# Kernel tuning notes

Measured on AMD Instinct MI355X. Metric: run time of the kernel, lower is better.

## Reference

```python
import jax, jax.numpy as jnp
import numpy as np

N_NODES = 50000
N_EDGES = 800000
IN_FEAT = 128
HEADS = 4
UNITS = 16
LEAKY_ALPHA = 0.2  # tf.nn.leaky_relu default


def setup_inputs() -> dict:
    key = jax.random.key(0)
    k1, k2, k3, k4, k5 = jax.random.split(key, 5)
    x = jax.random.normal(k1, (N_NODES, IN_FEAT), dtype=jnp.float32)
    edge_index = jax.random.randint(k2, (N_EDGES, 2), 0, N_NODES, dtype=jnp.int32)
    # Dense kernel (glorot-ish scaling), no bias (use_bias=False)
    W = jax.random.normal(k3, (IN_FEAT, HEADS * UNITS), dtype=jnp.float32) * (1.0 / np.sqrt(IN_FEAT))
    glorot = np.sqrt(2.0 / (1 + UNITS)).astype(np.float32)
    att_w1 = jax.random.normal(k4, (HEADS, 1, UNITS), dtype=jnp.float32) * glorot
    att_w2 = jax.random.normal(k5, (HEADS, 1, UNITS), dtype=jnp.float32) * glorot
    return {"x": x, "edge_index": edge_index, "W": W, "att_w1": att_w1, "att_w2": att_w2}


def reference(x, edge_index, W, att_w1, att_w2):
    n_nodes = x.shape[0]
    h = x @ W  # [N, H*U]
    snd_idx = edge_index[:, 0]
    rcv_idx = edge_index[:, 1]
    # gather per-edge features, split into heads -> [H, E, U]
    sender = h[snd_idx].reshape(-1, HEADS, UNITS).transpose(1, 0, 2)
    receiver = h[rcv_idx].reshape(-1, HEADS, UNITS).transpose(1, 0, 2)
    # per-edge, per-head attention logits [H, E]
    att = jnp.sum(att_w1 * sender, axis=-1) + jnp.sum(att_w2 * receiver, axis=-1)
    att = jnp.where(att > 0, att, LEAKY_ALPHA * att)
    # segment softmax over receiver neighborhoods, per head
    seg_max = jax.vmap(lambda a: jax.ops.segment_max(a, rcv_idx, num_segments=n_nodes))(att)  # [H, N]
    e = jnp.exp(att - seg_max[:, rcv_idx])
    denom = jax.vmap(lambda a: jax.ops.segment_sum(a, rcv_idx, num_segments=n_nodes))(e)  # [H, N]
    alpha = e / denom[:, rcv_idx]  # [H, E]
    # weighted scatter-sum of sender features -> [H, N, U]
    out = jax.vmap(lambda v: jax.ops.segment_sum(v, rcv_idx, num_segments=n_nodes))(sender * alpha[:, :, None])
    # concat heads -> [N, H*U]; activation is None (identity)
    return out.transpose(1, 0, 2).reshape(n_nodes, HEADS * UNITS)
```

## Files before the change

### kernel.cpp

```cpp
#include <hip/hip_runtime.h>
#include <math.h>

#define N_NODES 50000
#define N_EDGES 800000
#define IN_FEAT 128
#define HEADS   4
#define UNITS   16
#define OUTF    64
#define LEAKY   0.2f

#define NB      196
#define BCAP    5120
#define GEMM_BLKS 782
#define A_BLOCKS  391
#define EPB     8

typedef __attribute__((ext_vector_type(8))) short bf16x8;
typedef __attribute__((ext_vector_type(4))) float f32x4;

__device__ __forceinline__ unsigned short f2bf(float f) {
    unsigned u = __float_as_uint(f);
    unsigned r = u + 0x7FFFu + ((u >> 16) & 1u);
    return (unsigned short)(r >> 16);
}

union SharedU {
    struct { unsigned short xl[64 * 136]; unsigned short wt[64 * 136]; } g;
    struct { int2 stage[2048]; int hist[256], s[256], excl[256],
             gbase[256], cur[256]; } a;
};

__global__ __launch_bounds__(256) void wt_prep(const float* __restrict__ W,
                                               unsigned short* __restrict__ Wt_g,
                                               int* __restrict__ bucket_cnt) {
    int idx = blockIdx.x * 256 + threadIdx.x;
    if (blockIdx.x == 0 && threadIdx.x < NB) bucket_cnt[threadIdx.x] = 0;
    if (idx < IN_FEAT * OUTF) {
        int k = idx >> 6, c = idx & 63;
        Wt_g[c * IN_FEAT + k] = f2bf(W[idx]);
    }
}

__global__ __launch_bounds__(256) void fused_gemm_bucketA(const float* __restrict__ x,
                                                          const unsigned short* __restrict__ Wt_g,
                                                          const float* __restrict__ w1,
                                                          const float* __restrict__ w2,
                                                          const int2* __restrict__ ei,
                                                          unsigned short* __restrict__ hg,
                                                          float* __restrict__ a1,
                                                          float* __restrict__ a2,
                                                          int* __restrict__ bucket_cnt,
                                                          int2* __restrict__ buckets) {
    __shared__ SharedU sh;
    const int t = threadIdx.x;

    if (blockIdx.x >= GEMM_BLKS) {
        const int e0 = (blockIdx.x - GEMM_BLKS) * 2048;
        sh.a.hist[t] = 0;
        __syncthreads();

        int2 ed[EPB]; int bk[EPB];
        #pragma unroll
        for (int j = 0; j < EPB; ++j) {
            int e = e0 + t + j * 256;
            if (e < N_EDGES) {
                ed[j] = ei[e];
                bk[j] = ed[j].y >> 8;
                atomicAdd(&sh.a.hist[bk[j]], 1);
            } else bk[j] = -1;
        }
        __syncthreads();
        int v = sh.a.hist[t];
        sh.a.s[t] = v;
        __syncthreads();
        #pragma unroll
        for (int off = 1; off < 256; off <<= 1) {
            int u = (t >= off) ? sh.a.s[t - off] : 0;
            __syncthreads();
            sh.a.s[t] += u;
            __syncthreads();
        }
        sh.a.excl[t] = sh.a.s[t] - v;
        sh.a.cur[t] = 0;
        if (t < NB) sh.a.gbase[t] = atomicAdd(&bucket_cnt[t], v);
        __syncthreads();
        #pragma unroll
        for (int j = 0; j < EPB; ++j) {
            if (bk[j] >= 0) {
                int p = sh.a.excl[bk[j]] + atomicAdd(&sh.a.cur[bk[j]], 1);
                sh.a.stage[p] = ed[j];
            }
        }
        __syncthreads();
        const int total = min(2048, N_EDGES - e0);
        for (int i = t; i < total; i += 256) {
            int2 vv = sh.a.stage[i];
            int b = vv.y >> 8;
            buckets[(size_t)b * BCAP + sh.a.gbase[b] + (i - sh.a.excl[b])] = vv;
        }
        return;
    }

    const int node0 = blockIdx.x * 64;
    unsigned short* xl = sh.g.xl;
    unsigned short* wt = sh.g.wt;

    #pragma unroll
    for (int it = 0; it < 8; ++it) {
        int idx = t + 256 * it;
        int r = idx >> 5, q = idx & 31;
        int node = node0 + r;
        float4 v = make_float4(0.f, 0.f, 0.f, 0.f);
        if (node < N_NODES) v = *(const float4*)(x + (size_t)node * IN_FEAT + q * 4);
        ushort4 b;
        b.x = f2bf(v.x); b.y = f2bf(v.y); b.z = f2bf(v.z); b.w = f2bf(v.w);
        *(ushort4*)&xl[r * 136 + q * 4] = b;
    }
    {
        const ushort4* Wt4 = (const ushort4*)Wt_g;
        #pragma unroll
        for (int it = 0; it < 8; ++it) {
            int idx = t + 256 * it;
            int c = idx >> 5, u = idx & 31;
            *(ushort4*)&wt[c * 136 + u * 4] = Wt4[idx];
        }
    }
    __syncthreads();

    const int lane = t & 63, wv = t >> 6;
    const int m = lane & 15, quad = lane >> 4;
    const int n0 = wv * 16;

    f32x4 acc[4] = {{0,0,0,0},{0,0,0,0},{0,0,0,0},{0,0,0,0}};
    #pragma unroll
    for (int kc = 0; kc < 4; ++kc) {
        bf16x8 af = *(bf16x8*)&xl[(n0 + m) * 136 + kc * 32 + quad * 8];
        #pragma unroll
        for (int ct = 0; ct < 4; ++ct) {
            bf16x8 bfr = *(bf16x8*)&wt[(ct * 16 + m) * 136 + kc * 32 + quad * 8];
            acc[ct] = __builtin_amdgcn_mfma_f32_16x16x32_bf16(af, bfr, acc[ct], 0, 0, 0);
        }
    }

    #pragma unroll
    for (int ct = 0; ct < 4; ++ct) {
        const float u1 = w1[ct * 16 + m];
        const float u2 = w2[ct * 16 + m];
        #pragma unroll
        for (int r = 0; r < 4; ++r) {
            float p1 = acc[ct][r] * u1;
            float p2 = acc[ct][r] * u2;
            p1 += __shfl_xor(p1, 1, 64); p1 += __shfl_xor(p1, 2, 64);
            p1 += __shfl_xor(p1, 4, 64); p1 += __shfl_xor(p1, 8, 64);
            p2 += __shfl_xor(p2, 1, 64); p2 += __shfl_xor(p2, 2, 64);
            p2 += __shfl_xor(p2, 4, 64); p2 += __shfl_xor(p2, 8, 64);
            if (m == 0) {
                int node = node0 + n0 + quad * 4 + r;
                if (node < N_NODES) {
                    a1[node * 4 + ct] = p1;
                    a2[node * 4 + ct] = p2;
                }
            }
        }
    }

    __syncthreads();
    unsigned short* hl = sh.g.xl;
    #pragma unroll
    for (int ct = 0; ct < 4; ++ct)
        #pragma unroll
        for (int r = 0; r < 4; ++r)
            hl[(n0 + quad * 4 + r) * 72 + ct * 16 + m] = f2bf(acc[ct][r]);
    __syncthreads();
    #pragma unroll
    for (int it = 0; it < 2; ++it) {
        int u = t + 256 * it;
        int r = u >> 3, cg = u & 7;
        int node = node0 + r;
        if (node < N_NODES)
            *(uint4*)&hg[(size_t)node * OUTF + cg * 8] = *(uint4*)&hl[r * 72 + cg * 8];
    }
}

__global__ __launch_bounds__(256) void bucketB(const int2* __restrict__ buckets,
                                               const int* __restrict__ bucket_cnt,
                                               int* __restrict__ edge_snd,
                                               int* __restrict__ rs,
                                               int* __restrict__ re) {
    __shared__ int hist[256], cur[256], s[256];
    __shared__ int snds[BCAP];
    const int b = blockIdx.x;
    const int t = threadIdx.x;
    const int cnt = bucket_cnt[b];
    hist[t] = 0;
    __syncthreads();
    for (int i = t; i < cnt; i += 256)
        atomicAdd(&hist[buckets[(size_t)b * BCAP + i].y & 255], 1);
    __syncthreads();
    int v = hist[t];
    s[t] = v;
    __syncthreads();
    #pragma unroll
    for (int off = 1; off < 256; off <<= 1) {
        int u = (t >= off) ? s[t - off] : 0;
        __syncthreads();
        s[t] += u;
        __syncthreads();
    }
    const int excl = s[t] - v;
    cur[t] = excl;
    const int node = b * 256 + t;
    if (node < N_NODES) {
        rs[node] = b * BCAP + excl;
        re[node] = b * BCAP + excl + v;
    }
    __syncthreads();
    for (int i = t; i < cnt; i += 256) {
        int2 vv = buckets[(size_t)b * BCAP + i];
        int p = atomicAdd(&cur[vv.y & 255], 1);
        snds[p] = vv.x;
    }
    __syncthreads();
    for (int i = t; i < cnt; i += 256) edge_snd[(size_t)b * BCAP + i] = snds[i];
}

__global__ __launch_bounds__(256, 8) void gather_kernel(const int* __restrict__ rs,
                                                        const int* __restrict__ re,
                                                        const int* __restrict__ edge_snd,
                                                        const float* __restrict__ a1,
                                                        const float* __restrict__ a2,
                                                        const unsigned short* __restrict__ h,
                                                        float* __restrict__ out) {
    const int wave = threadIdx.x >> 6;
    const int lane = threadIdx.x & 63;
    const int n = blockIdx.x * 4 + wave;
    if (n >= N_NODES) return;
    const int sub  = lane >> 3;
    const int li   = lane & 7;
    const int head = li >> 1;
    const int base = rs[n];
    const int end  = re[n];
    if (end <= base) {
        if (sub == 0) {
            *(float4*)(out + (size_t)n * OUTF + li * 8)     = make_float4(0.f, 0.f, 0.f, 0.f);
            *(float4*)(out + (size_t)n * OUTF + li * 8 + 4) = make_float4(0.f, 0.f, 0.f, 0.f);
        }
        return;
    }
    const float a2h = a2[n * 4 + head];
    const uint4* h4 = (const uint4*)h;

    float acc[8] = {0.f,0.f,0.f,0.f,0.f,0.f,0.f,0.f};
    float den = 0.f;

    for (int i = base; i < end; i += 16) {
        #pragma unroll
        for (int g = 0; g < 2; ++g) {
            int eraw = i + g * 8 + sub;
            int eidx = min(eraw, end - 1);
            int s = edge_snd[eidx];
            float t0 = a1[s * 4 + head] + a2h;
            t0 = t0 > 0.f ? t0 : LEAKY * t0;
            float e = (eraw < end) ? __expf(t0) : 0.f;
            uint4 hv = h4[(unsigned)(s * 8 + li)];
            const unsigned hw[4] = {hv.x, hv.y, hv.z, hv.w};
            #pragma unroll
            for (int q = 0; q < 4; ++q) {
                acc[q*2+0] = fmaf(e, __uint_as_float(hw[q] << 16),         acc[q*2+0]);
                acc[q*2+1] = fmaf(e, __uint_as_float(hw[q] & 0xFFFF0000u), acc[q*2+1]);
            }
            den += e;
        }
    }

    #pragma unroll
    for (int off = 8; off <= 32; off <<= 1) {
        #pragma unroll
        for (int q = 0; q < 8; ++q) acc[q] += __shfl_xor(acc[q], off, 64);
        den += __shfl_xor(den, off, 64);
    }

    if (sub == 0) {
        float inv = 1.f / den;
        *(float4*)(out + (size_t)n * OUTF + li * 8) =
            make_float4(acc[0] * inv, acc[1] * inv, acc[2] * inv, acc[3] * inv);
        *(float4*)(out + (size_t)n * OUTF + li * 8 + 4) =
            make_float4(acc[4] * inv, acc[5] * inv, acc[6] * inv, acc[7] * inv);
    }
}

extern "C" void kernel_launch(void* const* d_in, const int* in_sizes, int n_in,
                              void* d_out, int out_size, void* d_ws, size_t ws_size,
                              hipStream_t stream) {
    const float* x  = (const float*)d_in[0];
    const int2*  ei = (const int2*)d_in[1];
    const float* W  = (const float*)d_in[2];
    const float* w1 = (const float*)d_in[3];
    const float* w2 = (const float*)d_in[4];
    float* out = (float*)d_out;

    unsigned short* h = (unsigned short*)d_ws;
    float* a1         = (float*)(h + (size_t)N_NODES * OUTF);
    float* a2         = a1 + (size_t)N_NODES * HEADS;
    int2*  buckets    = (int2*)(a2 + (size_t)N_NODES * HEADS);
    int*   edge_snd   = (int*)(buckets + (size_t)NB * BCAP);
    int*   rs         = edge_snd + (size_t)NB * BCAP;
    int*   re         = rs + N_NODES;
    int*   bucket_cnt = re + N_NODES;
    unsigned short* Wt_g = (unsigned short*)(bucket_cnt + NB);

    wt_prep<<<32, 256, 0, stream>>>(W, Wt_g, bucket_cnt);
    fused_gemm_bucketA<<<GEMM_BLKS + A_BLOCKS, 256, 0, stream>>>(x, Wt_g, w1, w2, ei,
                                                                 h, a1, a2,
                                                                 bucket_cnt, buckets);
    bucketB<<<NB, 256, 0, stream>>>(buckets, bucket_cnt, edge_snd, rs, re);
    gather_kernel<<<(N_NODES + 3) / 4, 256, 0, stream>>>(rs, re, edge_snd, a1, a2, h, out);
}
```

Before: 135.6 us.

## Replace bucket sort and CSR gather with per-bucket LDS atomic accumulation

Drops the bucketB counting-sort kernel and the per-node CSR gather kernel. A single kernel now runs one 1024-thread block per 256-node bucket, reads the unsorted edges of that bucket, and accumulates exp-weighted sender features and denominators into shared memory with float atomics before normalising and writing the output. This removes one launch and the sort pass along with its global traffic. In exchange it relies on many LDS float atomics, uses only 196 blocks (low occupancy across the GPU), and makes the floating-point summation order nondeterministic.

```diff
diff --git a/kernel.cpp b/kernel.cpp
--- a/kernel.cpp
+++ b/kernel.cpp
@@ -182,110 +182,62 @@
     }
 }
 
-__global__ __launch_bounds__(256) void bucketB(const int2* __restrict__ buckets,
-                                               const int* __restrict__ bucket_cnt,
-                                               int* __restrict__ edge_snd,
-                                               int* __restrict__ rs,
-                                               int* __restrict__ re) {
-    __shared__ int hist[256], cur[256], s[256];
-    __shared__ int snds[BCAP];
+__global__ __launch_bounds__(1024, 2) void gather_lds(const int2* __restrict__ buckets,
+                                                      const int* __restrict__ bucket_cnt,
+                                                      const float* __restrict__ a1,
+                                                      const float* __restrict__ a2,
+                                                      const unsigned short* __restrict__ h,
+                                                      float* __restrict__ out) {
+    __shared__ float oacc[256 * 68];
+    __shared__ float dsum[256 * 4];
+    __shared__ float a2l[1024];
     const int b = blockIdx.x;
     const int t = threadIdx.x;
     const int cnt = bucket_cnt[b];
-    hist[t] = 0;
-    __syncthreads();
-    for (int i = t; i < cnt; i += 256)
-        atomicAdd(&hist[buckets[(size_t)b * BCAP + i].y & 255], 1);
-    __syncthreads();
-    int v = hist[t];
-    s[t] = v;
-    __syncthreads();
-    #pragma unroll
-    for (int off = 1; off < 256; off <<= 1) {
-        int u = (t >= off) ? s[t - off] : 0;
-        __syncthreads();
-        s[t] += u;
-        __syncthreads();
-    }
-    const int excl = s[t] - v;
-    cur[t] = excl;
-    const int node = b * 256 + t;
-    if (node < N_NODES) {
-        rs[node] = b * BCAP + excl;
-        re[node] = b * BCAP + excl + v;
-    }
-    __syncthreads();
-    for (int i = t; i < cnt; i += 256) {
-        int2 vv = buckets[(size_t)b * BCAP + i];
-        int p = atomicAdd(&cur[vv.y & 255], 1);
-        snds[p] = vv.x;
-    }
-    __syncthreads();
-    for (int i = t; i < cnt; i += 256) edge_snd[(size_t)b * BCAP + i] = snds[i];
-}
-
-__global__ __launch_bounds__(256, 8) void gather_kernel(const int* __restrict__ rs,
-                                                        const int* __restrict__ re,
-                                                        const int* __restrict__ edge_snd,
-                                                        const float* __restrict__ a1,
-                                                        const float* __restrict__ a2,
-                                                        const unsigned short* __restrict__ h,
-                                                        float* __restrict__ out) {
-    const int wave = threadIdx.x >> 6;
-    const int lane = threadIdx.x & 63;
-    const int n = blockIdx.x * 4 + wave;
-    if (n >= N_NODES) return;
+
+    for (int i = t; i < 256 * 68; i += 1024) oacc[i] = 0.f;
+    dsum[t] = 0.f;
+    {
+        int gi = b * 1024 + t;
+        a2l[t] = (gi < N_NODES * HEADS) ? a2[gi] : 0.f;
+    }
+    __syncthreads();
+
+    const int lane = t & 63;
+    const int wv   = t >> 6;
     const int sub  = lane >> 3;
     const int li   = lane & 7;
     const int head = li >> 1;
-    const int base = rs[n];
-    const int end  = re[n];
-    if (end <= base) {
-        if (sub == 0) {
-            *(float4*)(out + (size_t)n * OUTF + li * 8)     = make_float4(0.f, 0.f, 0.f, 0.f);
-            *(float4*)(out + (size_t)n * OUTF + li * 8 + 4) = make_float4(0.f, 0.f, 0.f, 0.f);
-        }
-        return;
-    }
-    const float a2h = a2[n * 4 + head];
     const uint4* h4 = (const uint4*)h;
-
-    float acc[8] = {0.f,0.f,0.f,0.f,0.f,0.f,0.f,0.f};
-    float den = 0.f;
-
-    for (int i = base; i < end; i += 16) {
-        #pragma unroll
-        for (int g = 0; g < 2; ++g) {
-            int eraw = i + g * 8 + sub;
-            int eidx = min(eraw, end - 1);
-            int s = edge_snd[eidx];
-            float t0 = a1[s * 4 + head] + a2h;
-            t0 = t0 > 0.f ? t0 : LEAKY * t0;
-            float e = (eraw < end) ? __expf(t0) : 0.f;
-            uint4 hv = h4[(unsigned)(s * 8 + li)];
-            const unsigned hw[4] = {hv.x, hv.y, hv.z, hv.w};
-            #pragma unroll
-            for (int q = 0; q < 4; ++q) {
-                acc[q*2+0] = fmaf(e, __uint_as_float(hw[q] << 16),         acc[q*2+0]);
-                acc[q*2+1] = fmaf(e, __uint_as_float(hw[q] & 0xFFFF0000u), acc[q*2+1]);
-            }
-            den += e;
-        }
-    }
-
-    #pragma unroll
-    for (int off = 8; off <= 32; off <<= 1) {
-        #pragma unroll
-        for (int q = 0; q < 8; ++q) acc[q] += __shfl_xor(acc[q], off, 64);
-        den += __shfl_xor(den, off, 64);
-    }
-
-    if (sub == 0) {
-        float inv = 1.f / den;
-        *(float4*)(out + (size_t)n * OUTF + li * 8) =
-            make_float4(acc[0] * inv, acc[1] * inv, acc[2] * inv, acc[3] * inv);
-        *(float4*)(out + (size_t)n * OUTF + li * 8 + 4) =
-            make_float4(acc[4] * inv, acc[5] * inv, acc[6] * inv, acc[7] * inv);
+    const int2* bptr = buckets + (size_t)b * BCAP;
+
+    for (int i = wv * 8 + sub; i < cnt; i += 128) {
+        int2 ed = bptr[i];
+        int row = ed.y & 255;
+        float t0 = a1[ed.x * 4 + head] + a2l[row * 4 + head];
+        t0 = t0 > 0.f ? t0 : LEAKY * t0;
+        float e = __expf(t0);
+        uint4 hv = h4[(unsigned)(ed.x * 8 + li)];
+        const unsigned hw[4] = {hv.x, hv.y, hv.z, hv.w};
+        float* orow = &oacc[row * 68 + li * 8];
+        #pragma unroll
+        for (int q = 0; q < 4; ++q) {
+            atomicAdd(&orow[q * 2 + 0], e * __uint_as_float(hw[q] << 16));
+            atomicAdd(&orow[q * 2 + 1], e * __uint_as_float(hw[q] & 0xFFFF0000u));
+        }
+        if ((li & 1) == 0) atomicAdd(&dsum[row * 4 + head], e);
+    }
+    __syncthreads();
+
+    for (int u = t; u < 256 * 16; u += 1024) {
+        int r = u >> 4, g = u & 15;
+        int node = b * 256 + r;
+        if (node >= N_NODES) continue;
+        float dv = dsum[r * 4 + (g >> 2)];
+        float inv = dv > 0.f ? 1.f / dv : 0.f;
+        const float* orow = &oacc[r * 68 + g * 4];
+        *(float4*)(out + (size_t)node * OUTF + g * 4) =
+            make_float4(orow[0] * inv, orow[1] * inv, orow[2] * inv, orow[3] * inv);
     }
 }
 
@@ -303,16 +255,12 @@
     float* a1         = (float*)(h + (size_t)N_NODES * OUTF);
     float* a2         = a1 + (size_t)N_NODES * HEADS;
     int2*  buckets    = (int2*)(a2 + (size_t)N_NODES * HEADS);
-    int*   edge_snd   = (int*)(buckets + (size_t)NB * BCAP);
-    int*   rs         = edge_snd + (size_t)NB * BCAP;
-    int*   re         = rs + N_NODES;
-    int*   bucket_cnt = re + N_NODES;
+    int*   bucket_cnt = (int*)(buckets + (size_t)NB * BCAP);
     unsigned short* Wt_g = (unsigned short*)(bucket_cnt + NB);
 
     wt_prep<<<32, 256, 0, stream>>>(W, Wt_g, bucket_cnt);
     fused_gemm_bucketA<<<GEMM_BLKS + A_BLOCKS, 256, 0, stream>>>(x, Wt_g, w1, w2, ei,
                                                                  h, a1, a2,
                                                                  bucket_cnt, buckets);
-    bucketB<<<NB, 256, 0, stream>>>(buckets, bucket_cnt, edge_snd, rs, re);
-    gather_kernel<<<(N_NODES + 3) / 4, 256, 0, stream>>>(rs, re, edge_snd, a1, a2, h, out);
-}
+    gather_lds<<<NB, 1024, 0, stream>>>(buckets, bucket_cnt, a1, a2, h, out);
+}
```

Result: slower. 467.0 us (+244.4%).
